# Kernel optimization log

Hardware: AMD Instinct MI355X
Metric: run time of the kernel (lower is better)

Reference implementation:

```python
import jax, jax.numpy as jnp
import numpy as np

N, D, K = 262144, 64, 64
TEMPERATURE = 1.0
PRIOR_P = 0.1
PRIOR_LOGVAR0 = -2.0  # prior_logvar_0 buffer (constant per-dim)
LOG2PI = float(np.log(2.0 * np.pi))


def setup_inputs() -> dict:
    key = jax.random.key(0)
    k1, k2, k3, k4 = jax.random.split(key, 4)
    prior_phi_probs = jnp.full((D,), PRIOR_P, dtype=jnp.float32)
    phi_logits = jnp.log(prior_phi_probs / (1.0 - prior_phi_probs))  # init = prior log-odds
    return {
        "X": jax.random.normal(k1, (N, D), dtype=jnp.float32),
        "u_noise": jax.random.uniform(k2, (D,), dtype=jnp.float32),
        "phi_logits": phi_logits,
        "q_mu": jax.random.normal(k3, (K, D), dtype=jnp.float32),
        "q_logvar": jnp.full((K, D), -1.0, dtype=jnp.float32),
        "pi_logits": jnp.ones((K,), dtype=jnp.float32),
        "prior_phi_probs": prior_phi_probs,
    }


def reference(X, u_noise, phi_logits, q_mu, q_logvar, pi_logits, prior_phi_probs):
    n = X.shape[0]
    # Gumbel-sigmoid sample of phi (per-dimension gate), shape (D,)
    gumbel = -jnp.log(-jnp.log(u_noise + 1e-9) + 1e-9)
    phi = jax.nn.sigmoid((phi_logits + gumbel) / TEMPERATURE)

    logvar = jnp.clip(q_logvar, -5.0, 5.0)            # (K, D)
    inv_var = jnp.exp(-logvar)                        # (K, D)

    # sum_d phi_d * log N(x_d | mu_kd, var_kd), decomposed to GEMM form so the
    # full (N, K, D) tensor is never materialized:
    #   -0.5 * [ sum_d phi*(LOG2PI + logvar_kd)  +  sum_d phi*(x-mu)^2/var_kd ]
    a = phi[None, :] * inv_var                        # (K, D)
    quad = (jnp.einsum('nd,kd->nk', X * X, a)
            - 2.0 * jnp.einsum('nd,kd->nk', X, q_mu * a)
            + jnp.sum(q_mu * q_mu * a, axis=1)[None, :])          # (N, K)
    const_k = jnp.sum(phi[None, :] * (LOG2PI + logvar), axis=1)   # (K,)
    lp_cluster = -0.5 * (const_k[None, :] + quad)                 # (N, K)

    # background term: sum_d (1-phi_d) * log N(x_d | 0, exp(prior_logvar_0)); per-sample scalar
    inv_var0 = float(np.exp(-PRIOR_LOGVAR0))
    lp_bg = -0.5 * jnp.sum((1.0 - phi)[None, :]
                           * (LOG2PI + PRIOR_LOGVAR0 + X * X * inv_var0), axis=1)  # (N,)

    log_p_x_given_z = lp_cluster + lp_bg[:, None]     # (N, K)

    pi = jax.nn.softmax(pi_logits)
    log_joint = log_p_x_given_z + jnp.log(pi + 1e-9)[None, :]
    log_likelihood = jnp.sum(jax.nn.logsumexp(log_joint, axis=1))

    q_phi = jnp.clip(jax.nn.sigmoid(phi_logits), 1e-6, 1.0 - 1e-6)
    p_phi = jnp.clip(prior_phi_probs, 1e-6, 1.0 - 1e-6)
    kl_phi = jnp.sum(q_phi * (jnp.log(q_phi) - jnp.log(p_phi))
                     + (1.0 - q_phi) * (jnp.log(1.0 - q_phi) - jnp.log(1.0 - p_phi))) * n

    loss = -log_likelihood + kl_phi
    return (loss, q_phi, log_p_x_given_z)
```

## Files before the change

### kernel.cpp

```cpp
#include <hip/hip_runtime.h>
#include <hip/hip_bf16.h>
#include <math.h>

#define N_SAMPLES 262144
#define DDIM 64
#define KDIM 64
#define NBLOCKS 2048
#define NPART (NBLOCKS * 4)

#define LOG2PI 1.8378770664093453f
#define PRIOR_LV0 -2.0f
#define IV0 7.389056098930650f


#define WS_C     4096
#define WS_LPI   4160
#define WS_PART  4224

typedef __attribute__((ext_vector_type(8))) short short8;
typedef __attribute__((ext_vector_type(4))) float floatx4;

static __device__ inline unsigned short f2bf_bits(float f) {
  union { float f; unsigned u; } v; v.f = f;
  unsigned r = v.u + 0x7fffu + ((v.u >> 16) & 1u);
  return (unsigned short)(r >> 16);
}

__global__ __launch_bounds__(256) void setup_frags(
    const float* __restrict__ u_noise, const float* __restrict__ phi_logits,
    const float* __restrict__ q_mu, const float* __restrict__ q_logvar,
    const float* __restrict__ pi_logits, float* __restrict__ ws) {
  __shared__ float sPhi[DDIM];
  __shared__ float sR[DDIM];
  __shared__ float sBeta;
  __shared__ float sPart[4][KDIM];
  int tid = threadIdx.x;

  if (tid < 64) {
    int d = tid;
    float u = u_noise[d];
    float g = -__logf(-__logf(u + 1e-9f) + 1e-9f);
    float phi = 1.0f / (1.0f + __expf(-(phi_logits[d] + g)));
    sPhi[d] = phi;
    sR[d] = -0.5f * (1.0f - phi) * IV0;

    float betap = -0.5f * (1.0f - phi) * (LOG2PI + PRIOR_LV0);
    #pragma unroll
    for (int o = 1; o < 64; o <<= 1) betap += __shfl_xor(betap, o, 64);
    if (d == 0) sBeta = betap;

    float l = pi_logits[d];
    float m = l;
    #pragma unroll
    for (int o = 1; o < 64; o <<= 1) m = fmaxf(m, __shfl_xor(m, o, 64));
    float e = __expf(l - m);
    float s = e;
    #pragma unroll
    for (int o = 1; o < 64; o <<= 1) s += __shfl_xor(s, o, 64);
    ws[WS_LPI + d] = __logf(e / s + 1e-9f);
  }
  __syncthreads();

  {
    int k = tid & 63, seg = tid >> 6;
    const float* lvp = q_logvar + k * DDIM + seg * 16;
    const float* mup = q_mu + k * DDIM + seg * 16;
    float ap = 0.0f;
    #pragma unroll
    for (int dd = 0; dd < 16; ++dd) {
      int d = seg * 16 + dd;
      float lv = fminf(fmaxf(lvp[dd], -5.0f), 5.0f);
      float mu = mup[dd];
      ap += sPhi[d] * (LOG2PI + lv) + mu * mu * sPhi[d] * __expf(-lv);
    }
    sPart[seg][k] = ap;
  }

  unsigned short* bsw = (unsigned short*)ws;
  #pragma unroll
  for (int p = 0; p < 4; ++p) {
    int pr = p * 256 + tid;
    int s = pr >> 6, l = pr & 63;
    int kc = s >> 2, tl = s & 3, q = l >> 4, nn = l & 15;
    int k = tl * 16 + nn;
    int dbase = (kc & 1) * 32 + q * 8;
    const float* lvp = q_logvar + k * DDIM + dbase;
    float4 lv0 = *(const float4*)lvp;
    float4 lv1 = *(const float4*)(lvp + 4);
    float lvv[8] = {lv0.x, lv0.y, lv0.z, lv0.w, lv1.x, lv1.y, lv1.z, lv1.w};
    short r8[8];
    if (kc < 2) {
      #pragma unroll
      for (int j = 0; j < 8; ++j) {
        int d = dbase + j;
        float lv = fminf(fmaxf(lvv[j], -5.0f), 5.0f);
        r8[j] = (short)f2bf_bits(-0.5f * sPhi[d] * __expf(-lv) + sR[d]);
      }
    } else {
      const float* mup = q_mu + k * DDIM + dbase;
      float4 mu0 = *(const float4*)mup;
      float4 mu1 = *(const float4*)(mup + 4);
      float muv[8] = {mu0.x, mu0.y, mu0.z, mu0.w, mu1.x, mu1.y, mu1.z, mu1.w};
      #pragma unroll
      for (int j = 0; j < 8; ++j) {
        int d = dbase + j;
        float lv = fminf(fmaxf(lvv[j], -5.0f), 5.0f);
        r8[j] = (short)f2bf_bits(muv[j] * sPhi[d] * __expf(-lv));
      }
    }
    ((short8*)bsw)[pr] = (short8){r8[0], r8[1], r8[2], r8[3],
                                  r8[4], r8[5], r8[6], r8[7]};
  }

  __syncthreads();
  if (tid < 64) {
    float alpha = sPart[0][tid] + sPart[1][tid] + sPart[2][tid] + sPart[3][tid];
    ws[WS_C + tid] = -0.5f * alpha + sBeta;
  }
}

__global__ __launch_bounds__(256, 4) void gmm_main(
    const float* __restrict__ X, const float* __restrict__ ws,
    float* __restrict__ out) {
  int tid  = threadIdx.x;
  int lane = tid & 63;
  int w    = tid >> 6;
  int n    = lane & 15;
  int q    = lane >> 4;
  long wbase = ((long)blockIdx.x * 4 + w) * 32;

  const float* xr0 = X + (wbase + n) * DDIM;
  const float* xr1 = xr0 + 16 * DDIM;
  float4 raw[2][4];
  raw[0][0] = *(const float4*)(xr0 + q * 8);
  raw[0][1] = *(const float4*)(xr0 + q * 8 + 4);
  raw[0][2] = *(const float4*)(xr0 + 32 + q * 8);
  raw[0][3] = *(const float4*)(xr0 + 32 + q * 8 + 4);
  raw[1][0] = *(const float4*)(xr1 + q * 8);
  raw[1][1] = *(const float4*)(xr1 + q * 8 + 4);
  raw[1][2] = *(const float4*)(xr1 + 32 + q * 8);
  raw[1][3] = *(const float4*)(xr1 + 32 + q * 8 + 4);

  float cb[4], lpi[4];
  #pragma unroll
  for (int t = 0; t < 4; ++t) {
    cb[t]  = ws[WS_C + t * 16 + n];
    lpi[t] = ws[WS_LPI + t * 16 + n];
  }

  const short8* Bf = (const short8*)ws;
  float* lp = out + 1 + DDIM;
  float rowacc = 0.0f;

  #pragma unroll
  for (int tt = 0; tt < 2; ++tt) {
    long rbase = wbase + tt * 16;
    short8 a[4];
    {
      float xa[8] = {raw[tt][0].x, raw[tt][0].y, raw[tt][0].z, raw[tt][0].w,
                     raw[tt][1].x, raw[tt][1].y, raw[tt][1].z, raw[tt][1].w};
      float xb[8] = {raw[tt][2].x, raw[tt][2].y, raw[tt][2].z, raw[tt][2].w,
                     raw[tt][3].x, raw[tt][3].y, raw[tt][3].z, raw[tt][3].w};
      #pragma unroll
      for (int j = 0; j < 8; ++j) {
        a[0][j] = (short)f2bf_bits(xa[j] * xa[j]);
        a[1][j] = (short)f2bf_bits(xb[j] * xb[j]);
        a[2][j] = (short)f2bf_bits(xa[j]);
        a[3][j] = (short)f2bf_bits(xb[j]);
      }
    }
    floatx4 acc[4];
    #pragma unroll
    for (int t = 0; t < 4; ++t) acc[t] = (floatx4){0.f, 0.f, 0.f, 0.f};
    #pragma unroll
    for (int kc = 0; kc < 4; ++kc) {
      #pragma unroll
      for (int t = 0; t < 4; ++t) {
        short8 b = Bf[(kc * 4 + t) * 64 + lane];
        acc[t] = __builtin_amdgcn_mfma_f32_16x16x32_bf16(a[kc], b, acc[t], 0, 0, 0);
      }
    }
    #pragma unroll
    for (int reg = 0; reg < 4; ++reg) {
      long row = rbase + q * 4 + reg;
      float o0 = acc[0][reg] + cb[0];
      float o1 = acc[1][reg] + cb[1];
      float o2 = acc[2][reg] + cb[2];
      float o3 = acc[3][reg] + cb[3];
      long off = row * KDIM + n;
      lp[off]      = o0;
      lp[off + 16] = o1;
      lp[off + 32] = o2;
      lp[off + 48] = o3;
      float v0 = o0 + lpi[0], v1 = o1 + lpi[1], v2 = o2 + lpi[2], v3 = o3 + lpi[3];
      float m = fmaxf(fmaxf(v0, v1), fmaxf(v2, v3));
      #pragma unroll
      for (int o = 1; o <= 8; o <<= 1) m = fmaxf(m, __shfl_xor(m, o, 64));
      float s = __expf(v0 - m) + __expf(v1 - m) + __expf(v2 - m) + __expf(v3 - m);
      #pragma unroll
      for (int o = 1; o <= 8; o <<= 1) s += __shfl_xor(s, o, 64);
      if (n == 0) rowacc += m + __logf(s);
    }
  }

  float t2 = (n == 0) ? rowacc : 0.0f;
  t2 += __shfl_xor(t2, 16, 64);
  t2 += __shfl_xor(t2, 32, 64);
  if (lane == 0) {
    float* wsp = (float*)ws;
    wsp[WS_PART + blockIdx.x * 4 + w] = t2;
  }
}

__global__ __launch_bounds__(256) void finalize_kernel(
    const float* __restrict__ phi_logits, const float* __restrict__ prior_p,
    const float* __restrict__ ws, float* __restrict__ out) {
  __shared__ float sW[4];
  __shared__ float sKl;
  int tid = threadIdx.x;
  int lane = tid & 63, w = tid >> 6;

  float s = 0.0f;
  #pragma unroll
  for (int i = 0; i < NPART / 256; ++i)
    s += ws[WS_PART + i * 256 + tid];
  #pragma unroll
  for (int o = 1; o < 64; o <<= 1) s += __shfl_xor(s, o, 64);
  if (lane == 0) sW[w] = s;

  if (tid < 64) {
    int d = tid;
    float qp = 1.0f / (1.0f + __expf(-phi_logits[d]));
    qp = fminf(fmaxf(qp, 1e-6f), 1.0f - 1e-6f);
    out[1 + d] = qp;
    float pp = fminf(fmaxf(prior_p[d], 1e-6f), 1.0f - 1e-6f);
    float klp = qp * (__logf(qp) - __logf(pp)) +
                (1.0f - qp) * (__logf(1.0f - qp) - __logf(1.0f - pp));
    #pragma unroll
    for (int o = 1; o < 64; o <<= 1) klp += __shfl_xor(klp, o, 64);
    if (d == 0) sKl = klp * (float)N_SAMPLES;
  }
  __syncthreads();
  if (tid == 0) out[0] = sKl - (sW[0] + sW[1] + sW[2] + sW[3]);
}

extern "C" void kernel_launch(void* const* d_in, const int* in_sizes, int n_in,
                              void* d_out, int out_size, void* d_ws, size_t ws_size,
                              hipStream_t stream) {
  const float* X           = (const float*)d_in[0];
  const float* u_noise     = (const float*)d_in[1];
  const float* phi_logits  = (const float*)d_in[2];
  const float* q_mu        = (const float*)d_in[3];
  const float* q_logvar    = (const float*)d_in[4];
  const float* pi_logits   = (const float*)d_in[5];
  const float* prior_p     = (const float*)d_in[6];
  float* out = (float*)d_out;
  float* ws  = (float*)d_ws;

  setup_frags<<<1, 256, 0, stream>>>(u_noise, phi_logits, q_mu, q_logvar,
                                     pi_logits, ws);
  gmm_main<<<NBLOCKS, 256, 0, stream>>>(X, ws, out);
  finalize_kernel<<<1, 256, 0, stream>>>(phi_logits, prior_p, ws, out);
}
```

Before: 144.0 us.

## Halve rows per wave, double occupancy, and use DPP row reductions

The main kernel now has each wave process 16 rows instead of 32. It launches twice as many blocks and raises the launch-bounds occupancy hint from 4 to 8 blocks per CU, aiming for more memory-level parallelism. The per-row logsumexp max/sum reductions within 16-lane rows use DPP row rotations instead of ds_swizzle/shuffle. The q_phi/KL computation moves from finalize into the setup kernel, shortening the serial tail. The trade-off is less per-wave work to hide latency and more partial sums for finalize to read.

```diff
diff --git a/kernel.cpp b/kernel.cpp
--- a/kernel.cpp
+++ b/kernel.cpp
@@ -5,7 +5,7 @@
 #define N_SAMPLES 262144
 #define DDIM 64
 #define KDIM 64
-#define NBLOCKS 2048
+#define NBLOCKS 4096
 #define NPART (NBLOCKS * 4)
 
 #define LOG2PI 1.8378770664093453f
@@ -16,9 +16,13 @@
 #define WS_C     4096
 #define WS_LPI   4160
 #define WS_PART  4224
+#define WS_KL    (WS_PART + NPART)
 
 typedef __attribute__((ext_vector_type(8))) short short8;
 typedef __attribute__((ext_vector_type(4))) float floatx4;
+
+#define DPP_ROR(v, N) __int_as_float(__builtin_amdgcn_update_dpp( \
+    0, __float_as_int(v), 0x120 + (N), 0xf, 0xf, false))
 
 static __device__ inline unsigned short f2bf_bits(float f) {
   union { float f; unsigned u; } v; v.f = f;
@@ -29,7 +33,8 @@
 __global__ __launch_bounds__(256) void setup_frags(
     const float* __restrict__ u_noise, const float* __restrict__ phi_logits,
     const float* __restrict__ q_mu, const float* __restrict__ q_logvar,
-    const float* __restrict__ pi_logits, float* __restrict__ ws) {
+    const float* __restrict__ pi_logits, const float* __restrict__ prior_p,
+    float* __restrict__ out, float* __restrict__ ws) {
   __shared__ float sPhi[DDIM];
   __shared__ float sR[DDIM];
   __shared__ float sBeta;
@@ -58,6 +63,17 @@
     #pragma unroll
     for (int o = 1; o < 64; o <<= 1) s += __shfl_xor(s, o, 64);
     ws[WS_LPI + d] = __logf(e / s + 1e-9f);
+  } else if (tid >= 64 && tid < 128) {
+    int d = tid - 64;
+    float qp = 1.0f / (1.0f + __expf(-phi_logits[d]));
+    qp = fminf(fmaxf(qp, 1e-6f), 1.0f - 1e-6f);
+    out[1 + d] = qp;
+    float pp = fminf(fmaxf(prior_p[d], 1e-6f), 1.0f - 1e-6f);
+    float klp = qp * (__logf(qp) - __logf(pp)) +
+                (1.0f - qp) * (__logf(1.0f - qp) - __logf(1.0f - pp));
+    #pragma unroll
+    for (int o = 1; o < 64; o <<= 1) klp += __shfl_xor(klp, o, 64);
+    if (d == 0) ws[WS_KL] = klp * (float)N_SAMPLES;
   }
   __syncthreads();
 
@@ -119,7 +135,7 @@
   }
 }
 
-__global__ __launch_bounds__(256, 4) void gmm_main(
+__global__ __launch_bounds__(256, 8) void gmm_main(
     const float* __restrict__ X, const float* __restrict__ ws,
     float* __restrict__ out) {
   int tid  = threadIdx.x;
@@ -127,19 +143,13 @@
   int w    = tid >> 6;
   int n    = lane & 15;
   int q    = lane >> 4;
-  long wbase = ((long)blockIdx.x * 4 + w) * 32;
-
-  const float* xr0 = X + (wbase + n) * DDIM;
-  const float* xr1 = xr0 + 16 * DDIM;
-  float4 raw[2][4];
-  raw[0][0] = *(const float4*)(xr0 + q * 8);
-  raw[0][1] = *(const float4*)(xr0 + q * 8 + 4);
-  raw[0][2] = *(const float4*)(xr0 + 32 + q * 8);
-  raw[0][3] = *(const float4*)(xr0 + 32 + q * 8 + 4);
-  raw[1][0] = *(const float4*)(xr1 + q * 8);
-  raw[1][1] = *(const float4*)(xr1 + q * 8 + 4);
-  raw[1][2] = *(const float4*)(xr1 + 32 + q * 8);
-  raw[1][3] = *(const float4*)(xr1 + 32 + q * 8 + 4);
+  long rbase = ((long)blockIdx.x * 4 + w) * 16;
+
+  const float* xr = X + (rbase + n) * DDIM;
+  float4 xa0 = *(const float4*)(xr + q * 8);
+  float4 xa1 = *(const float4*)(xr + q * 8 + 4);
+  float4 xb0 = *(const float4*)(xr + 32 + q * 8);
+  float4 xb1 = *(const float4*)(xr + 32 + q * 8 + 4);
 
   float cb[4], lpi[4];
   #pragma unroll
@@ -148,62 +158,60 @@
     lpi[t] = ws[WS_LPI + t * 16 + n];
   }
 
+  short8 a[4];
+  {
+    float xa[8] = {xa0.x, xa0.y, xa0.z, xa0.w, xa1.x, xa1.y, xa1.z, xa1.w};
+    float xb[8] = {xb0.x, xb0.y, xb0.z, xb0.w, xb1.x, xb1.y, xb1.z, xb1.w};
+    #pragma unroll
+    for (int j = 0; j < 8; ++j) {
+      a[0][j] = (short)f2bf_bits(xa[j] * xa[j]);
+      a[1][j] = (short)f2bf_bits(xb[j] * xb[j]);
+      a[2][j] = (short)f2bf_bits(xa[j]);
+      a[3][j] = (short)f2bf_bits(xb[j]);
+    }
+  }
+
   const short8* Bf = (const short8*)ws;
+  floatx4 acc[4];
+  #pragma unroll
+  for (int t = 0; t < 4; ++t) acc[t] = (floatx4){0.f, 0.f, 0.f, 0.f};
+  #pragma unroll
+  for (int kc = 0; kc < 4; ++kc) {
+    #pragma unroll
+    for (int t = 0; t < 4; ++t) {
+      short8 b = Bf[(kc * 4 + t) * 64 + lane];
+      acc[t] = __builtin_amdgcn_mfma_f32_16x16x32_bf16(a[kc], b, acc[t], 0, 0, 0);
+    }
+  }
+
   float* lp = out + 1 + DDIM;
   float rowacc = 0.0f;
-
-  #pragma unroll
-  for (int tt = 0; tt < 2; ++tt) {
-    long rbase = wbase + tt * 16;
-    short8 a[4];
-    {
-      float xa[8] = {raw[tt][0].x, raw[tt][0].y, raw[tt][0].z, raw[tt][0].w,
-                     raw[tt][1].x, raw[tt][1].y, raw[tt][1].z, raw[tt][1].w};
-      float xb[8] = {raw[tt][2].x, raw[tt][2].y, raw[tt][2].z, raw[tt][2].w,
-                     raw[tt][3].x, raw[tt][3].y, raw[tt][3].z, raw[tt][3].w};
-      #pragma unroll
-      for (int j = 0; j < 8; ++j) {
-        a[0][j] = (short)f2bf_bits(xa[j] * xa[j]);
-        a[1][j] = (short)f2bf_bits(xb[j] * xb[j]);
-        a[2][j] = (short)f2bf_bits(xa[j]);
-        a[3][j] = (short)f2bf_bits(xb[j]);
-      }
-    }
-    floatx4 acc[4];
-    #pragma unroll
-    for (int t = 0; t < 4; ++t) acc[t] = (floatx4){0.f, 0.f, 0.f, 0.f};
-    #pragma unroll
-    for (int kc = 0; kc < 4; ++kc) {
-      #pragma unroll
-      for (int t = 0; t < 4; ++t) {
-        short8 b = Bf[(kc * 4 + t) * 64 + lane];
-        acc[t] = __builtin_amdgcn_mfma_f32_16x16x32_bf16(a[kc], b, acc[t], 0, 0, 0);
-      }
-    }
-    #pragma unroll
-    for (int reg = 0; reg < 4; ++reg) {
-      long row = rbase + q * 4 + reg;
-      float o0 = acc[0][reg] + cb[0];
-      float o1 = acc[1][reg] + cb[1];
-      float o2 = acc[2][reg] + cb[2];
-      float o3 = acc[3][reg] + cb[3];
-      long off = row * KDIM + n;
-      lp[off]      = o0;
-      lp[off + 16] = o1;
-      lp[off + 32] = o2;
-      lp[off + 48] = o3;
-      float v0 = o0 + lpi[0], v1 = o1 + lpi[1], v2 = o2 + lpi[2], v3 = o3 + lpi[3];
-      float m = fmaxf(fmaxf(v0, v1), fmaxf(v2, v3));
-      #pragma unroll
-      for (int o = 1; o <= 8; o <<= 1) m = fmaxf(m, __shfl_xor(m, o, 64));
-      float s = __expf(v0 - m) + __expf(v1 - m) + __expf(v2 - m) + __expf(v3 - m);
-      #pragma unroll
-      for (int o = 1; o <= 8; o <<= 1) s += __shfl_xor(s, o, 64);
-      if (n == 0) rowacc += m + __logf(s);
-    }
-  }
-
-  float t2 = (n == 0) ? rowacc : 0.0f;
+  #pragma unroll
+  for (int reg = 0; reg < 4; ++reg) {
+    long row = rbase + q * 4 + reg;
+    float o0 = acc[0][reg] + cb[0];
+    float o1 = acc[1][reg] + cb[1];
+    float o2 = acc[2][reg] + cb[2];
+    float o3 = acc[3][reg] + cb[3];
+    long off = row * KDIM + n;
+    lp[off]      = o0;
+    lp[off + 16] = o1;
+    lp[off + 32] = o2;
+    lp[off + 48] = o3;
+    float v0 = o0 + lpi[0], v1 = o1 + lpi[1], v2 = o2 + lpi[2], v3 = o3 + lpi[3];
+    float m = fmaxf(fmaxf(v0, v1), fmaxf(v2, v3));
+    m = fmaxf(m, DPP_ROR(m, 8));
+    m = fmaxf(m, DPP_ROR(m, 4));
+    m = fmaxf(m, DPP_ROR(m, 2));
+    m = fmaxf(m, DPP_ROR(m, 1));
+    float s = __expf(v0 - m) + __expf(v1 - m) + __expf(v2 - m) + __expf(v3 - m);
+    s += DPP_ROR(s, 8);
+    s += DPP_ROR(s, 4);
+    s += DPP_ROR(s, 2);
+    s += DPP_ROR(s, 1);
+    rowacc += m + __logf(s);
+  }
+  float t2 = rowacc;
   t2 += __shfl_xor(t2, 16, 64);
   t2 += __shfl_xor(t2, 32, 64);
   if (lane == 0) {
@@ -213,10 +221,8 @@
 }
 
 __global__ __launch_bounds__(256) void finalize_kernel(
-    const float* __restrict__ phi_logits, const float* __restrict__ prior_p,
     const float* __restrict__ ws, float* __restrict__ out) {
   __shared__ float sW[4];
-  __shared__ float sKl;
   int tid = threadIdx.x;
   int lane = tid & 63, w = tid >> 6;
 
@@ -227,21 +233,8 @@
   #pragma unroll
   for (int o = 1; o < 64; o <<= 1) s += __shfl_xor(s, o, 64);
   if (lane == 0) sW[w] = s;
-
-  if (tid < 64) {
-    int d = tid;
-    float qp = 1.0f / (1.0f + __expf(-phi_logits[d]));
-    qp = fminf(fmaxf(qp, 1e-6f), 1.0f - 1e-6f);
-    out[1 + d] = qp;
-    float pp = fminf(fmaxf(prior_p[d], 1e-6f), 1.0f - 1e-6f);
-    float klp = qp * (__logf(qp) - __logf(pp)) +
-                (1.0f - qp) * (__logf(1.0f - qp) - __logf(1.0f - pp));
-    #pragma unroll
-    for (int o = 1; o < 64; o <<= 1) klp += __shfl_xor(klp, o, 64);
-    if (d == 0) sKl = klp * (float)N_SAMPLES;
-  }
   __syncthreads();
-  if (tid == 0) out[0] = sKl - (sW[0] + sW[1] + sW[2] + sW[3]);
+  if (tid == 0) out[0] = ws[WS_KL] - (sW[0] + sW[1] + sW[2] + sW[3]);
 }
 
 extern "C" void kernel_launch(void* const* d_in, const int* in_sizes, int n_in,
@@ -258,7 +251,7 @@
   float* ws  = (float*)d_ws;
 
   setup_frags<<<1, 256, 0, stream>>>(u_noise, phi_logits, q_mu, q_logvar,
-                                     pi_logits, ws);
+                                     pi_logits, prior_p, out, ws);
   gmm_main<<<NBLOCKS, 256, 0, stream>>>(X, ws, out);
-  finalize_kernel<<<1, 256, 0, stream>>>(phi_logits, prior_p, ws, out);
-}
+  finalize_kernel<<<1, 256, 0, stream>>>(ws, out);
+}
```

Result: faster. 140.7 us (-2.3%).
